# Optimization experiments

Measured on AMD Instinct MI355X. Metric: run time of the kernel, lower is better.

## Reference

```python
import jax, jax.numpy as jnp
import numpy as np

N_ATOMS = 20000
N_EDGES = 640000
N_TRIP = 2000000
CHANNELS = 128
EXP_FEAT = 64
CUTOFF = 5.0


def _gated_mlp(x, W1, W2, G1, G2):
    # mlp: Linear -> SiLU -> Linear ; gate: Linear -> SiLU -> Linear -> Sigmoid
    main = jax.nn.silu(x @ W1) @ W2
    gate = jax.nn.sigmoid(jax.nn.silu(x @ G1) @ G2)
    return main * gate


def setup_inputs() -> dict:
    key = jax.random.key(0)
    ks = jax.random.split(key, 20)
    inp = {}
    inp['features'] = jax.random.normal(ks[0], (N_ATOMS, CHANNELS), jnp.float32)
    inp['neighbour_distances'] = jax.random.uniform(ks[1], (N_EDGES,), jnp.float32) * CUTOFF
    inp['angles'] = jax.random.uniform(ks[2], (N_TRIP,), jnp.float32) * np.pi
    inp['r_ij'] = jax.random.uniform(ks[3], (N_TRIP,), jnp.float32) * CUTOFF
    inp['r_ik'] = jax.random.uniform(ks[4], (N_TRIP,), jnp.float32) * CUTOFF
    inp['neighbour_list'] = jax.random.randint(ks[5], (2, N_EDGES), 0, N_ATOMS)
    inp['triplet_idxs'] = jax.random.randint(ks[6], (N_TRIP, 3), 0, N_ATOMS)

    def w(k, fan_in, shape):
        return jax.random.normal(k, shape, jnp.float32) / np.sqrt(fan_in)

    inp['W_pre'] = w(ks[7], CHANNELS, (CHANNELS, CHANNELS))
    inp['tb_W1'] = w(ks[8], EXP_FEAT, (EXP_FEAT, EXP_FEAT))
    inp['tb_W2'] = w(ks[9], EXP_FEAT, (EXP_FEAT, CHANNELS))
    inp['tb_G1'] = w(ks[10], EXP_FEAT, (EXP_FEAT, EXP_FEAT))
    inp['tb_G2'] = w(ks[11], EXP_FEAT, (EXP_FEAT, CHANNELS))
    inp['th_W1'] = w(ks[12], 3, (3, 64))
    inp['th_W2'] = w(ks[13], 64, (64, CHANNELS))
    inp['th_G1'] = w(ks[14], 3, (3, 64))
    inp['th_G2'] = w(ks[15], 64, (64, CHANNELS))
    inp['W_post'] = w(ks[16], CHANNELS, (CHANNELS, CHANNELS))
    return inp


def reference(features, neighbour_distances, angles, r_ij, r_ik,
              neighbour_list, triplet_idxs,
              W_pre, tb_W1, tb_W2, tb_G1, tb_G2,
              th_W1, th_W2, th_G1, th_G2, W_post):
    n_atoms, channels = features.shape
    n_edges = neighbour_distances.shape[0]

    # 1. pre-linear
    h = features @ W_pre  # [n_atoms, C]

    # 2. radial basis (Gaussian smearing) with smooth cosine cutoff envelope
    centers = jnp.linspace(0.0, CUTOFF, EXP_FEAT, dtype=features.dtype)
    sigma = CUTOFF / EXP_FEAT
    d = neighbour_distances[:, None]  # [n_edges, 1]
    rb = jnp.exp(-((d - centers) ** 2) / (2.0 * sigma * sigma))  # [n_edges, E]
    cutoff_mask = (neighbour_distances < CUTOFF).astype(features.dtype)
    cutoff_values = 0.5 * (1.0 + jnp.cos(np.pi * neighbour_distances / CUTOFF))
    rb = rb * (cutoff_values * cutoff_mask)[:, None]

    # 3. two-body messages: gather neighbour features, modulate by gated MLP of rb
    neighbor_h = h[neighbour_list[1]]  # [n_edges, C]
    two_body = neighbor_h * _gated_mlp(rb, tb_W1, tb_W2, tb_G1, tb_G2)

    # 4. three-body messages (replicates torch index_add into [n_edges, C] buffer
    #    using the triplet atom-index column, as in the original code)
    f3 = jnp.stack([r_ij, r_ik, jnp.cos(angles)], axis=-1)  # [n_trip, 3]
    w3 = _gated_mlp(f3, th_W1, th_W2, th_G1, th_G2)  # [n_trip, C]
    msgs = h[triplet_idxs[:, 1]] * w3  # [n_trip, C]
    three_body = jnp.zeros((n_edges, channels), features.dtype).at[triplet_idxs[:, 1]].add(msgs)

    # 5. aggregate messages to central atoms, then post-linear
    messages = two_body + three_body  # [n_edges, C]
    h_out = jax.ops.segment_sum(messages, neighbour_list[0], num_segments=n_atoms)
    return h_out @ W_post
```

## Files before the change

kernel.cpp:

```cpp
#include <hip/hip_runtime.h>
#include <hip/hip_fp16.h>

#define NAT 20000
#define NE  640000
#define NT  2000000
#define CH  128
#define EF  64
#define NB  4096
#define PI_F 3.14159265358979f
#define NLOG2E (-1.44269504088896f)

#define CAP_T 160
#define CAP_E 72

#define G_SC2  2048
#define G_GEMM 625
#define G_LUT  2049
#define G_FB   1024

typedef __attribute__((ext_vector_type(8))) __bf16 bf16x8;
typedef __attribute__((ext_vector_type(4))) float floatx4;
typedef __attribute__((ext_vector_type(2))) float floatx2;

__device__ __forceinline__ float fsigmoid(float x) {
    return __builtin_amdgcn_rcpf(1.0f + __expf(-x));
}
__device__ __forceinline__ float fsilu(float x) { return x * fsigmoid(x); }

__device__ __forceinline__ floatx2 fsigmoid2(floatx2 x) {
    floatx2 nx = x * NLOG2E;
    floatx2 e = {__builtin_amdgcn_exp2f(nx.x), __builtin_amdgcn_exp2f(nx.y)};
    floatx2 d = e + 1.0f;
    return floatx2{__builtin_amdgcn_rcpf(d.x), __builtin_amdgcn_rcpf(d.y)};
}
__device__ __forceinline__ floatx2 fsilu2(floatx2 x) { return x * fsigmoid2(x); }

__global__ __launch_bounds__(256) void gemm128(const float* __restrict__ X,
                                               const float* __restrict__ W,
                                               float* __restrict__ Y) {
    __shared__ float Xs[32 * 128];
    __shared__ float Ws[32 * 128];
    int tid = threadIdx.x;
    int row0 = blockIdx.x * 32;

    const float4* Xg = (const float4*)(X + (size_t)row0 * 128);
    float4* Xs4 = (float4*)Xs;
#pragma unroll
    for (int i = 0; i < 4; ++i) Xs4[tid + 256 * i] = Xg[tid + 256 * i];

    int r0 = (tid >> 5) << 2;
    int c0 = (tid & 31) << 2;
    floatx4 acc[4];
#pragma unroll
    for (int i = 0; i < 4; ++i) acc[i] = floatx4{0.f, 0.f, 0.f, 0.f};

    for (int kb = 0; kb < 4; ++kb) {
        __syncthreads();
        const float4* Wg = (const float4*)(W + kb * 32 * 128);
        float4* Ws4 = (float4*)Ws;
#pragma unroll
        for (int i = 0; i < 4; ++i) Ws4[tid + 256 * i] = Wg[tid + 256 * i];
        __syncthreads();
#pragma unroll
        for (int kk = 0; kk < 32; ++kk) {
            int k = kb * 32 + kk;
            floatx4 wv = *(const floatx4*)&Ws[kk * 128 + c0];
            float x0 = Xs[(r0 + 0) * 128 + k];
            float x1 = Xs[(r0 + 1) * 128 + k];
            float x2 = Xs[(r0 + 2) * 128 + k];
            float x3 = Xs[(r0 + 3) * 128 + k];
            acc[0] += x0 * wv;
            acc[1] += x1 * wv;
            acc[2] += x2 * wv;
            acc[3] += x3 * wv;
        }
    }
#pragma unroll
    for (int i = 0; i < 4; ++i)
        *(floatx4*)&Y[(size_t)(row0 + r0 + i) * 128 + c0] = acc[i];
}

__global__ __launch_bounds__(256) void mid2(const int* __restrict__ tri,
                                            const int* __restrict__ nl,
                                            const float* __restrict__ rij,
                                            const float* __restrict__ rik,
                                            const float* __restrict__ ang,
                                            const float* __restrict__ dist,
                                            int* __restrict__ tcur, int* __restrict__ ecur,
                                            float2* __restrict__ tdP,
                                            unsigned* __restrict__ edP,
                                            const float* __restrict__ X,
                                            const float* __restrict__ W,
                                            float* __restrict__ Y,
                                            const float* __restrict__ W1,
                                            const float* __restrict__ W2,
                                            const float* __restrict__ G1,
                                            const float* __restrict__ G2,
                                            float* __restrict__ lut) {
    __shared__ float Xs[32 * 128];
    __shared__ float Ws[32 * 128];
    int bid = blockIdx.x, tid = threadIdx.x;

    if (bid < G_SC2) {
        const int NT4 = NT / 4, NE4 = NE / 4;
        int stride = G_SC2 * 256;
        for (int grp = bid * 256 + tid; grp < NT4 + NE4; grp += stride) {
            if (grp < NT4) {
                int g = grp << 2;
                int4 t0 = *(const int4*)&tri[(size_t)g * 3];
                int4 t1 = *(const int4*)&tri[(size_t)g * 3 + 4];
                int4 t2 = *(const int4*)&tri[(size_t)g * 3 + 8];
                float4 rj = *(const float4*)&rij[g];
                float4 rk = *(const float4*)&rik[g];
                float4 an = *(const float4*)&ang[g];
                int   cc[4] = {t0.y, t1.x, t1.w, t2.z};
                float rjv[4] = {rj.x, rj.y, rj.z, rj.w};
                float rkv[4] = {rk.x, rk.y, rk.z, rk.w};
                float anv[4] = {an.x, an.y, an.z, an.w};
#pragma unroll
                for (int u = 0; u < 4; ++u) {
                    int p = atomicAdd(&tcur[cc[u]], 1);
                    if (p < CAP_T) {
                        unsigned lo = __half_as_ushort(__float2half_rn(rjv[u]));
                        unsigned hi = __half_as_ushort(__float2half_rn(rkv[u]));
                        tdP[(size_t)cc[u] * CAP_T + p] =
                            make_float2(__uint_as_float(lo | (hi << 16)), __cosf(anv[u]));
                    }
                }
            } else {
                int e = (grp - NT4) << 2;
                int4 cc4 = *(const int4*)&nl[e];
                float4 dd = *(const float4*)&dist[e];
                int4 ii = *(const int4*)&nl[NE + e];
                int   cc[4] = {cc4.x, cc4.y, cc4.z, cc4.w};
                float ddv[4] = {dd.x, dd.y, dd.z, dd.w};
                int   iiv[4] = {ii.x, ii.y, ii.z, ii.w};
#pragma unroll
                for (int u = 0; u < 4; ++u) {
                    int p = atomicAdd(&ecur[cc[u]], 1);
                    if (p < CAP_E) {
                        unsigned dq = (unsigned)(ddv[u] * 13107.0f + 0.5f);
                        edP[cc[u] * CAP_E + p] = dq | ((unsigned)iiv[u] << 16);
                    }
                }
            }
        }
    } else if (bid < G_SC2 + G_GEMM) {
        int row0 = (bid - G_SC2) * 32;
        const float4* Xg = (const float4*)(X + (size_t)row0 * 128);
        float4* Xs4 = (float4*)Xs;
#pragma unroll
        for (int i = 0; i < 4; ++i) Xs4[tid + 256 * i] = Xg[tid + 256 * i];
        int r0 = (tid >> 5) << 2;
        int c0 = (tid & 31) << 2;
        floatx4 acc[4];
#pragma unroll
        for (int i = 0; i < 4; ++i) acc[i] = floatx4{0.f, 0.f, 0.f, 0.f};
        for (int kb = 0; kb < 4; ++kb) {
            __syncthreads();
            const float4* Wg = (const float4*)(W + kb * 32 * 128);
            float4* Ws4 = (float4*)Ws;
#pragma unroll
            for (int i = 0; i < 4; ++i) Ws4[tid + 256 * i] = Wg[tid + 256 * i];
            __syncthreads();
#pragma unroll
            for (int kk = 0; kk < 32; ++kk) {
                int k = kb * 32 + kk;
                floatx4 wv = *(const floatx4*)&Ws[kk * 128 + c0];
                float x0 = Xs[(r0 + 0) * 128 + k];
                float x1 = Xs[(r0 + 1) * 128 + k];
                float x2 = Xs[(r0 + 2) * 128 + k];
                float x3 = Xs[(r0 + 3) * 128 + k];
                acc[0] += x0 * wv;
                acc[1] += x1 * wv;
                acc[2] += x2 * wv;
                acc[3] += x3 * wv;
            }
        }
#pragma unroll
        for (int i = 0; i < 4; ++i)
            *(floatx4*)&Y[(size_t)(row0 + r0 + i) * 128 + c0] = acc[i];
    } else {
        float* rb = Xs;
        float* hm = Xs + 128;
        float* hg = Xs + 256;
        int half = tid >> 7, t = tid & 127;
        int p = (bid - G_SC2 - G_GEMM) * 2 + half;
        bool live = (p <= NB);
        float d = p * (5.0f / NB);
        if (live && t < 64) {
            float ctr = t * (5.0f / 63.0f);
            float sig = 5.0f / 64.0f;
            float z = (d - ctr);
            float g = __expf(-z * z / (2.0f * sig * sig));
            float env = (d < 5.0f) ? 0.5f * (1.0f + __cosf(PI_F * d / 5.0f)) : 0.0f;
            rb[half * 64 + t] = g * env;
        }
        __syncthreads();
        if (live) {
            int j = t & 63;
            const float* Wm = (t < 64) ? W1 : G1;
            float s = 0.0f;
            for (int k = 0; k < 64; ++k) s += rb[half * 64 + k] * Wm[k * 64 + j];
            float hv = fsilu(s);
            if (t < 64) hm[half * 64 + j] = hv; else hg[half * 64 + j] = hv;
        }
        __syncthreads();
        if (live) {
            float m = 0.0f, g = 0.0f;
            for (int j = 0; j < 64; ++j) {
                m += hm[half * 64 + j] * W2[j * 128 + t];
                g += hg[half * 64 + j] * G2[j * 128 + t];
            }
            lut[(size_t)p * 128 + t] = m * fsigmoid(g);
        }
    }
}

__global__ __launch_bounds__(256) void fused_bodies(const float2* __restrict__ tdP,
                                                    const unsigned* __restrict__ edP,
                                                    const int* __restrict__ tcur,
                                                    const int* __restrict__ ecur,
                                                    const float* __restrict__ h,
                                                    const float* __restrict__ lut,
                                                    const float* __restrict__ thW1,
                                                    const float* __restrict__ thW2,
                                                    const float* __restrict__ thG1,
                                                    const float* __restrict__ thG2,
                                                    const int* __restrict__ nl,
                                                    float* __restrict__ acc) {
    __shared__ __bf16 lw2[64 * 128];
    __shared__ __bf16 lg2[64 * 128];
    __shared__ float lw1[192];
    __shared__ float lg1[192];
    int tid = threadIdx.x;
    for (int i = tid; i < 192; i += 256) { lw1[i] = thW1[i]; lg1[i] = thG1[i]; }
    for (int e = tid; e < 64 * 128; e += 256) {
        int k = e >> 7, c = e & 127;
        int tile = c >> 4, n = c & 15, s = k >> 5, q = (k >> 3) & 3, j = k & 7;
        int li = ((((tile << 1) + s) * 64) + (q << 4) + n) * 8 + j;
        lw2[li] = (__bf16)thW2[e];
        lg2[li] = (__bf16)thG2[e];
    }
    __syncthreads();

    int lane = tid & 63;
    int q = lane >> 4, n = lane & 15;
    int lfrag = ((q << 4) + n) << 3;
    int c2 = lane << 1;
    int wid = (blockIdx.x << 2) + (tid >> 6);
    int nw = gridDim.x << 2;

    for (int a = wid; a < NAT; a += nw) {
        int dst = nl[a];
        float hrow[8];
        if (q == 0) {
#pragma unroll
            for (int t = 0; t < 8; ++t) hrow[t] = h[(size_t)a * 128 + (t << 4) + n];
        }

        {
            int base = a * CAP_T;
            int cnt = tcur[a]; if (cnt > CAP_T) cnt = CAP_T;
            floatx2 accT[8];
#pragma unroll
            for (int t = 0; t < 8; ++t) accT[t] = floatx2{0.f, 0.f};

            for (int i0 = 0; i0 < cnt; i0 += 64) {
                int rem = cnt - i0;
                float tx = 0.f, ty = 0.f, tz = 0.f;
                if (lane < rem) {
                    float2 p = tdP[base + i0 + lane];
                    unsigned bits = __float_as_uint(p.x);
                    tx = __half2float(__ushort_as_half((unsigned short)(bits & 0xffff)));
                    ty = __half2float(__ushort_as_half((unsigned short)(bits >> 16)));
                    tz = p.y;
                }
                float rrv[4], kkv[4], ccv[4];
#pragma unroll
                for (int ms = 0; ms < 4; ++ms) {
                    rrv[ms] = __shfl(tx, (ms << 4) + n);
                    kkv[ms] = __shfl(ty, (ms << 4) + n);
                    ccv[ms] = __shfl(tz, (ms << 4) + n);
                }
                int nms = rem >= 64 ? 4 : ((rem + 15) >> 4);

                bf16x8 fam[4][2], fag[4][2];
#pragma unroll
                for (int s = 0; s < 2; ++s) {
                    int kb = s * 32 + (q << 3);
#pragma unroll
                    for (int j2 = 0; j2 < 4; ++j2) {
                        floatx2 wa0 = *(const floatx2*)&lw1[kb + 2 * j2];
                        floatx2 wa1 = *(const floatx2*)&lw1[64 + kb + 2 * j2];
                        floatx2 wa2 = *(const floatx2*)&lw1[128 + kb + 2 * j2];
                        floatx2 wb0 = *(const floatx2*)&lg1[kb + 2 * j2];
                        floatx2 wb1 = *(const floatx2*)&lg1[64 + kb + 2 * j2];
                        floatx2 wb2 = *(const floatx2*)&lg1[128 + kb + 2 * j2];
#pragma unroll
                        for (int ms = 0; ms < 4; ++ms) {
                            if (ms >= nms) break;
                            floatx2 rr2 = {rrv[ms], rrv[ms]};
                            floatx2 kk2 = {kkv[ms], kkv[ms]};
                            floatx2 cc2 = {ccv[ms], ccv[ms]};
                            floatx2 um = rr2 * wa0 + kk2 * wa1 + cc2 * wa2;
                            floatx2 ug = rr2 * wb0 + kk2 * wb1 + cc2 * wb2;
                            floatx2 sm = fsilu2(um);
                            floatx2 sg = fsilu2(ug);
                            fam[ms][s][2 * j2]     = (__bf16)sm.x;
                            fam[ms][s][2 * j2 + 1] = (__bf16)sm.y;
                            fag[ms][s][2 * j2]     = (__bf16)sg.x;
                            fag[ms][s][2 * j2 + 1] = (__bf16)sg.y;
                        }
                    }
                }

#pragma unroll
                for (int tile = 0; tile < 8; ++tile) {
                    __builtin_amdgcn_sched_barrier(0);
                    const __bf16* pw = lw2 + lfrag + tile * 1024;
                    const __bf16* pg = lg2 + lfrag + tile * 1024;
                    bf16x8 bw0 = *(const bf16x8*)(pw);
                    bf16x8 bw1 = *(const bf16x8*)(pw + 512);
                    bf16x8 bg0 = *(const bf16x8*)(pg);
                    bf16x8 bg1 = *(const bf16x8*)(pg + 512);
#pragma unroll
                    for (int ms = 0; ms < 4; ++ms) {
                        if (ms >= nms) break;
                        floatx4 am = {0.f, 0.f, 0.f, 0.f};
                        floatx4 ag = {0.f, 0.f, 0.f, 0.f};
                        am = __builtin_amdgcn_mfma_f32_16x16x32_bf16(fam[ms][0], bw0, am, 0, 0, 0);
                        am = __builtin_amdgcn_mfma_f32_16x16x32_bf16(fam[ms][1], bw1, am, 0, 0, 0);
                        ag = __builtin_amdgcn_mfma_f32_16x16x32_bf16(fag[ms][0], bg0, ag, 0, 0, 0);
                        ag = __builtin_amdgcn_mfma_f32_16x16x32_bf16(fag[ms][1], bg1, ag, 0, 0, 0);
                        floatx2 s01 = fsigmoid2(floatx2{ag[0], ag[1]});
                        floatx2 s23 = fsigmoid2(floatx2{ag[2], ag[3]});
                        accT[tile] += floatx2{am[0], am[1]} * s01
                                    + floatx2{am[2], am[3]} * s23;
                    }
                }
            }
#pragma unroll
            for (int tile = 0; tile < 8; ++tile) {
                float v = accT[tile].x + accT[tile].y;
                v += __shfl_xor(v, 16);
                v += __shfl_xor(v, 32);
                if (q == 0)
                    unsafeAtomicAdd(&acc[(size_t)dst * 128 + (tile << 4) + n], hrow[tile] * v);
            }
        }
        {
            int base = a * CAP_E;
            int cnt = ecur[a]; if (cnt > CAP_E) cnt = CAP_E;
            float s0 = 0.f, s1 = 0.f, t0 = 0.f, t1 = 0.f;
            for (int i0 = 0; i0 < cnt; i0 += 64) {
                int rem = cnt - i0; if (rem > 64) rem = 64;
                int ev = 0;
                if (lane < rem) ev = (int)edP[base + i0 + lane];
                int j = 0;
                for (; j + 2 <= rem; j += 2) {
                    unsigned evA = (unsigned)__shfl(ev, j);
                    unsigned evB = (unsigned)__shfl(ev, j + 1);
                    float dA = (float)(evA & 0xffff) * (1.0f / 13107.0f);
                    int aA = (int)(evA >> 16);
                    float dB = (float)(evB & 0xffff) * (1.0f / 13107.0f);
                    int aB = (int)(evB >> 16);
                    float xA = dA * ((float)NB / 5.0f);
                    int iA = (int)xA; if (iA > NB - 1) iA = NB - 1;
                    float fA = xA - (float)iA;
                    float xB = dB * ((float)NB / 5.0f);
                    int iB = (int)xB; if (iB > NB - 1) iB = NB - 1;
                    float fB = xB - (float)iB;
                    float2 l0A = *(const float2*)&lut[(size_t)iA * 128 + c2];
                    float2 l1A = *(const float2*)&lut[(size_t)(iA + 1) * 128 + c2];
                    float2 hvA = *(const float2*)&h[(size_t)aA * 128 + c2];
                    float2 l0B = *(const float2*)&lut[(size_t)iB * 128 + c2];
                    float2 l1B = *(const float2*)&lut[(size_t)(iB + 1) * 128 + c2];
                    float2 hvB = *(const float2*)&h[(size_t)aB * 128 + c2];
                    s0 += hvA.x * (l0A.x + (l1A.x - l0A.x) * fA);
                    s1 += hvA.y * (l0A.y + (l1A.y - l0A.y) * fA);
                    t0 += hvB.x * (l0B.x + (l1B.x - l0B.x) * fB);
                    t1 += hvB.y * (l0B.y + (l1B.y - l0B.y) * fB);
                }
                if (j < rem) {
                    unsigned evA = (unsigned)__shfl(ev, j);
                    float d = (float)(evA & 0xffff) * (1.0f / 13107.0f);
                    int a1 = (int)(evA >> 16);
                    float x = d * ((float)NB / 5.0f);
                    int i = (int)x; if (i > NB - 1) i = NB - 1;
                    float f = x - (float)i;
                    float2 l0 = *(const float2*)&lut[(size_t)i * 128 + c2];
                    float2 l1 = *(const float2*)&lut[(size_t)(i + 1) * 128 + c2];
                    float2 hv = *(const float2*)&h[(size_t)a1 * 128 + c2];
                    s0 += hv.x * (l0.x + (l1.x - l0.x) * f);
                    s1 += hv.y * (l0.y + (l1.y - l0.y) * f);
                }
            }
            unsafeAtomicAdd(&acc[(size_t)a * 128 + c2],     s0 + t0);
            unsafeAtomicAdd(&acc[(size_t)a * 128 + c2 + 1], s1 + t1);
        }
    }
}

extern "C" void kernel_launch(void* const* d_in, const int* in_sizes, int n_in,
                              void* d_out, int out_size, void* d_ws, size_t ws_size,
                              hipStream_t stream) {
    const float* features = (const float*)d_in[0];
    const float* dist = (const float*)d_in[1];
    const float* ang = (const float*)d_in[2];
    const float* rij = (const float*)d_in[3];
    const float* rik = (const float*)d_in[4];
    const int* nl = (const int*)d_in[5];
    const int* tri = (const int*)d_in[6];
    const float* W_pre = (const float*)d_in[7];
    const float* tbW1 = (const float*)d_in[8];
    const float* tbW2 = (const float*)d_in[9];
    const float* tbG1 = (const float*)d_in[10];
    const float* tbG2 = (const float*)d_in[11];
    const float* thW1 = (const float*)d_in[12];
    const float* thW2 = (const float*)d_in[13];
    const float* thG1 = (const float*)d_in[14];
    const float* thG2 = (const float*)d_in[15];
    const float* W_post = (const float*)d_in[16];
    float* out = (float*)d_out;

    float2* tdP   = (float2*)d_ws;
    unsigned* edP = (unsigned*)(tdP + (size_t)NAT * CAP_T);
    float* h   = (float*)(edP + (size_t)NAT * CAP_E);
    float* lut = h + (size_t)NAT * CH;
    int* tcur  = (int*)(lut + (size_t)(NB + 1) * CH);
    int* ecur  = tcur + NAT;
    float* acc = out;

    hipMemsetAsync(tcur, 0, (size_t)2 * NAT * sizeof(int), stream);
    hipMemsetAsync(acc, 0, (size_t)NAT * CH * sizeof(float), stream);

    mid2<<<G_SC2 + G_GEMM + G_LUT, 256, 0, stream>>>(
        tri, nl, rij, rik, ang, dist, tcur, ecur, tdP, edP,
        features, W_pre, h, tbW1, tbW2, tbG1, tbG2, lut);
    fused_bodies<<<G_FB, 256, 0, stream>>>(tdP, edP, tcur, ecur, h, lut,
                                           thW1, thW2, thG1, thG2, nl, acc);
    gemm128<<<NAT / 32, 256, 0, stream>>>(acc, W_post, out);
}
```

Measured before the change: 550.1 us.

## Split triplet/edge bucketing scatter into multiple passes by destination atom range

The bucketing loop now runs five passes over all triplets and edges, and each pass only handles destination atoms in one fifth of the index range. This is meant to keep the atomic counters and scattered writes in a cache-resident window. Payload values are loaded lazily only for in-range entries. The trade-off is reading the index arrays five times and losing vectorized payload loads.

```diff
diff --git a/kernel.cpp b/kernel.cpp
--- a/kernel.cpp
+++ b/kernel.cpp
@@ -12,6 +12,9 @@
 
 #define CAP_T 160
 #define CAP_E 72
+
+#define PASSES 5
+#define PRANGE (NAT / PASSES)
 
 #define G_SC2  2048
 #define G_GEMM 625
@@ -104,43 +107,43 @@
     if (bid < G_SC2) {
         const int NT4 = NT / 4, NE4 = NE / 4;
         int stride = G_SC2 * 256;
-        for (int grp = bid * 256 + tid; grp < NT4 + NE4; grp += stride) {
-            if (grp < NT4) {
-                int g = grp << 2;
-                int4 t0 = *(const int4*)&tri[(size_t)g * 3];
-                int4 t1 = *(const int4*)&tri[(size_t)g * 3 + 4];
-                int4 t2 = *(const int4*)&tri[(size_t)g * 3 + 8];
-                float4 rj = *(const float4*)&rij[g];
-                float4 rk = *(const float4*)&rik[g];
-                float4 an = *(const float4*)&ang[g];
-                int   cc[4] = {t0.y, t1.x, t1.w, t2.z};
-                float rjv[4] = {rj.x, rj.y, rj.z, rj.w};
-                float rkv[4] = {rk.x, rk.y, rk.z, rk.w};
-                float anv[4] = {an.x, an.y, an.z, an.w};
-#pragma unroll
-                for (int u = 0; u < 4; ++u) {
-                    int p = atomicAdd(&tcur[cc[u]], 1);
-                    if (p < CAP_T) {
-                        unsigned lo = __half_as_ushort(__float2half_rn(rjv[u]));
-                        unsigned hi = __half_as_ushort(__float2half_rn(rkv[u]));
-                        tdP[(size_t)cc[u] * CAP_T + p] =
-                            make_float2(__uint_as_float(lo | (hi << 16)), __cosf(anv[u]));
+        for (int pass = 0; pass < PASSES; ++pass) {
+            int lo = pass * PRANGE;
+            int hi = lo + PRANGE;
+            for (int grp = bid * 256 + tid; grp < NT4 + NE4; grp += stride) {
+                if (grp < NT4) {
+                    int g = grp << 2;
+                    int4 t0 = *(const int4*)&tri[(size_t)g * 3];
+                    int4 t1 = *(const int4*)&tri[(size_t)g * 3 + 4];
+                    int4 t2 = *(const int4*)&tri[(size_t)g * 3 + 8];
+                    int cc[4] = {t0.y, t1.x, t1.w, t2.z};
+#pragma unroll
+                    for (int u = 0; u < 4; ++u) {
+                        if (cc[u] >= lo && cc[u] < hi) {
+                            int p = atomicAdd(&tcur[cc[u]], 1);
+                            if (p < CAP_T) {
+                                unsigned lov = __half_as_ushort(__float2half_rn(rij[g + u]));
+                                unsigned hiv = __half_as_ushort(__float2half_rn(rik[g + u]));
+                                tdP[(size_t)cc[u] * CAP_T + p] =
+                                    make_float2(__uint_as_float(lov | (hiv << 16)),
+                                                __cosf(ang[g + u]));
+                            }
+                        }
                     }
-                }
-            } else {
-                int e = (grp - NT4) << 2;
-                int4 cc4 = *(const int4*)&nl[e];
-                float4 dd = *(const float4*)&dist[e];
-                int4 ii = *(const int4*)&nl[NE + e];
-                int   cc[4] = {cc4.x, cc4.y, cc4.z, cc4.w};
-                float ddv[4] = {dd.x, dd.y, dd.z, dd.w};
-                int   iiv[4] = {ii.x, ii.y, ii.z, ii.w};
-#pragma unroll
-                for (int u = 0; u < 4; ++u) {
-                    int p = atomicAdd(&ecur[cc[u]], 1);
-                    if (p < CAP_E) {
-                        unsigned dq = (unsigned)(ddv[u] * 13107.0f + 0.5f);
-                        edP[cc[u] * CAP_E + p] = dq | ((unsigned)iiv[u] << 16);
+                } else {
+                    int e = (grp - NT4) << 2;
+                    int4 cc4 = *(const int4*)&nl[e];
+                    int cc[4] = {cc4.x, cc4.y, cc4.z, cc4.w};
+#pragma unroll
+                    for (int u = 0; u < 4; ++u) {
+                        if (cc[u] >= lo && cc[u] < hi) {
+                            int p = atomicAdd(&ecur[cc[u]], 1);
+                            if (p < CAP_E) {
+                                unsigned dq = (unsigned)(dist[e + u] * 13107.0f + 0.5f);
+                                unsigned idx = (unsigned)nl[NE + e + u];
+                                edP[cc[u] * CAP_E + p] = dq | (idx << 16);
+                            }
+                        }
                     }
                 }
             }
```

New measurement: 550.4 us. Within noise of the previous version (+0.1%).
